# Kernel tuning notes

Hardware: AMD Instinct MI355X
Metric: run time of the kernel (lower is better)

Reference implementation:

```python
import jax, jax.numpy as jnp
import numpy as np

B, F, E, K, O = 4096, 64, 16, 8, 32
NFEAT, HID = 100000, 1024
EPS = 1e-5
N_ITER = 50  # entmax bisection iterations (entmax package default)


def entmax15(x):
    # alpha=1.5 entmax via bisection, faithful to EntmaxBisectFunction.forward
    d = x.shape[-1]
    xs = x * 0.5  # X * (alpha - 1)
    mx = jnp.max(xs, axis=-1, keepdims=True)
    tau_lo = mx - 1.0                      # gp(1, 1.5) = 1
    tau_hi = mx - (1.0 / d) ** 0.5         # gp(1/d, 1.5)
    f_lo = jnp.sum(jnp.square(jnp.maximum(xs - tau_lo, 0.0)), -1, keepdims=True) - 1.0
    dm = tau_hi - tau_lo

    def body(i, carry):
        tau_lo, dm, _ = carry
        dm = dm * 0.5
        tau_m = tau_lo + dm
        f_m = jnp.sum(jnp.square(jnp.maximum(xs - tau_m, 0.0)), -1, keepdims=True) - 1.0
        tau_lo = jnp.where(f_m * f_lo >= 0, tau_m, tau_lo)
        return (tau_lo, dm, tau_m)

    _, _, tau_m = jax.lax.fori_loop(0, N_ITER, body, (tau_lo, dm, tau_lo))
    p = jnp.square(jnp.maximum(xs - tau_m, 0.0))
    return p / jnp.sum(p, -1, keepdims=True)


def bn_channels(x, g, b):
    # BatchNorm1d on (B, C, L): normalize over batch and L per channel C (train mode)
    m = jnp.mean(x, (0, 2), keepdims=True)
    v = jnp.var(x, (0, 2), keepdims=True)
    return (x - m) / jnp.sqrt(v + EPS) * g[None, :, None] + b[None, :, None]


def bn_feat(x, g, b):
    # BatchNorm1d on (B, C) (train mode, biased variance)
    m = jnp.mean(x, 0)
    v = jnp.var(x, 0)
    return (x - m) / jnp.sqrt(v + EPS) * g + b


def setup_inputs() -> dict:
    key = jax.random.key(0)
    ks = jax.random.split(key, 12)
    gain = 1.414
    aQ = gain * np.sqrt(6.0 / (O + E))
    aB = gain * np.sqrt(6.0 / (E + E))
    aV = gain * np.sqrt(6.0 / (O + F))
    D0 = K * O * E
    return {
        'x_id': jax.random.randint(ks[0], (B, F), 0, NFEAT),
        'x_value': jax.random.uniform(ks[1], (B, F), dtype=jnp.float32),
        'emb': jax.random.normal(ks[2], (NFEAT, E), dtype=jnp.float32) * 0.1,
        'emb_g': jnp.ones((F,), jnp.float32), 'emb_b': jnp.zeros((F,), jnp.float32),
        'Q': jax.random.uniform(ks[3], (K, O, E), jnp.float32, -aQ, aQ),
        'bil': jax.random.uniform(ks[4], (K, E, E), jnp.float32, -aB, aB),
        'vals': jax.random.uniform(ks[5], (K, O, F), jnp.float32, -aV, aV),
        'arm_g': jnp.ones((K * O,), jnp.float32), 'arm_b': jnp.zeros((K * O,), jnp.float32),
        'w1': jax.random.normal(ks[6], (HID, D0), jnp.float32) / np.sqrt(D0),
        'b1': jnp.zeros((HID,), jnp.float32),
        'g1': jnp.ones((HID,), jnp.float32), 'bt1': jnp.zeros((HID,), jnp.float32),
        'w2': jax.random.normal(ks[7], (HID, HID), jnp.float32) / np.sqrt(HID),
        'b2': jnp.zeros((HID,), jnp.float32),
        'g2': jnp.ones((HID,), jnp.float32), 'bt2': jnp.zeros((HID,), jnp.float32),
        'wout': jax.random.normal(ks[8], (1, HID), jnp.float32) / np.sqrt(HID),
        'bout': jnp.zeros((1,), jnp.float32),
    }


def reference(x_id, x_value, emb, emb_g, emb_b, Q, bil, vals, arm_g, arm_b,
              w1, b1, g1, bt1, w2, b2, g2, bt2, wout, bout):
    v = jnp.clip(x_value, 0.001, 1.0)
    xe = emb[x_id] * v[..., None]                       # B,F,E
    x_exp = bn_channels(jnp.exp(xe), emb_g, emb_b)       # B,F,E
    # bilinear attention scores + global context bias
    kq = jnp.einsum('kxy,koy->kox', bil, Q)              # K,O,E (fuse param contraction)
    sc = jnp.einsum('bfx,kox->bkof', xe, kq)             # B,K,O,F
    gc = jnp.einsum('bx,kox->bko', xe.sum(1), kq)        # B,K,O
    sg = entmax15(sc + gc[..., None])                    # B,K,O,F sparse gates
    aw = sg * vals[None]                                 # B,K,O,F
    arm = jnp.einsum('bfe,bkof->bkoe', x_exp, aw)        # B,K,O,E
    arm = arm.reshape(arm.shape[0], K * O, E)
    arm = bn_channels(arm, arm_g, arm_b).reshape(arm.shape[0], -1)
    h = jax.nn.relu(bn_feat(arm @ w1.T + b1, g1, bt1))
    h = jax.nn.relu(bn_feat(h @ w2.T + b2, g2, bt2))
    y = h @ wout.T + bout
    return y[:, 0]
```

## Files before the change

### kernel.cpp

```cpp
#include <hip/hip_runtime.h>

#define EPS 1e-5f

typedef __bf16 bf16;
typedef bf16 bf16x8 __attribute__((ext_vector_type(8)));
typedef float f32x4 __attribute__((ext_vector_type(4)));
typedef float f32x2 __attribute__((ext_vector_type(2)));

__device__ __forceinline__ void lds_cp16(void* lds, const void* g) {
  __builtin_amdgcn_global_load_lds(
      (const __attribute__((address_space(1))) void*)g,
      (__attribute__((address_space(3))) void*)lds, 16, 0, 0);
}

__device__ __forceinline__ f32x4 mfma_bf16(bf16x8 a, bf16x8 b, f32x4 c) {
  return __builtin_amdgcn_mfma_f32_16x16x32_bf16(a, b, c, 0, 0, 0);
}

__global__ void k_zero(float* p) { p[blockIdx.x * 256 + threadIdx.x] = 0.0f; }

__global__ void k_embed(const int* __restrict__ x_id, const float* __restrict__ x_val,
                        const float* __restrict__ emb, float* __restrict__ xe) {
  int g = blockIdx.x * 256 + threadIdx.x;
  int id = x_id[g];
  float v = fminf(fmaxf(x_val[g], 0.001f), 1.0f);
  const float4* er = (const float4*)(emb + (size_t)id * 16);
  float4* xo = (float4*)(xe + (size_t)g * 16);
#pragma unroll
  for (int j = 0; j < 4; ++j) {
    float4 e = er[j];
    e.x *= v; e.y *= v; e.z *= v; e.w *= v;
    xo[j] = e;
  }
}

__global__ void k_expstats(const float* __restrict__ xe, float* __restrict__ es,
                           float* __restrict__ eq) {
  int t = threadIdx.x;
  int b0 = blockIdx.x * 16;
  float4 s4 = {0, 0, 0, 0}, q4 = {0, 0, 0, 0};
  for (int i = 0; i < 16; ++i) {
    float4 v = ((const float4*)(xe + (size_t)(b0 + i) * 1024))[t];
    float4 e;
    e.x = __expf(v.x); e.y = __expf(v.y); e.z = __expf(v.z); e.w = __expf(v.w);
    s4.x += e.x; s4.y += e.y; s4.z += e.z; s4.w += e.w;
    q4.x += e.x * e.x; q4.y += e.y * e.y; q4.z += e.z * e.z; q4.w += e.w * e.w;
  }
  float s = (s4.x + s4.y) + (s4.z + s4.w);
  float q = (q4.x + q4.y) + (q4.z + q4.w);
  s += __shfl_xor(s, 1, 64); s += __shfl_xor(s, 2, 64);
  q += __shfl_xor(q, 1, 64); q += __shfl_xor(q, 2, 64);
  if ((t & 3) == 0) {
    int f = t >> 2;
    atomicAdd(es + f, s);
    atomicAdd(eq + f, q);
  }
}

__global__ void k_expfin(const float* __restrict__ es, const float* __restrict__ eq,
                         const float* __restrict__ g_, const float* __restrict__ b_,
                         float* __restrict__ oa, float* __restrict__ ob) {
  int f = threadIdx.x;
  float mean = es[f] * (1.0f / 65536.0f);
  float var = eq[f] * (1.0f / 65536.0f) - mean * mean;
  float a = g_[f] * rsqrtf(var + EPS);
  oa[f] = a;
  ob[f] = b_[f] - mean * a;
}

__global__ void k_kq(const float* __restrict__ Qw, const float* __restrict__ bil,
                     float* __restrict__ kq) {
  int t = threadIdx.x;
  int k = t >> 5;
  float qv[16];
#pragma unroll
  for (int y = 0; y < 16; ++y) qv[y] = Qw[t * 16 + y];
  const float* bl = bil + k * 256;
#pragma unroll
  for (int x = 0; x < 16; ++x) {
    float s = 0.f;
#pragma unroll
    for (int y = 0; y < 16; ++y) s += bl[x * 16 + y] * qv[y];
    kq[t * 16 + x] = 0.5f * s;
  }
}

__global__ __launch_bounds__(256, 2) void k_attn(
    const float* __restrict__ xe_g, const float* __restrict__ kq_g,
    const float* __restrict__ eba, const float* __restrict__ ebb,
    const float* __restrict__ vals, bf16* __restrict__ arm) {
  __shared__ __align__(16) float s_xe[64 * 16];
  __shared__ float s_sum[16];
  __shared__ __align__(16) bf16 s_aw[256 * 72];
  __shared__ __align__(16) bf16 s_X[16 * 72];
  const int t = threadIdx.x;
  const int b = blockIdx.x;
  const f32x2 z2 = {0.f, 0.f};

  ((float4*)s_xe)[t] = ((const float4*)(xe_g + (size_t)b * 1024))[t];
  __syncthreads();

  if (t < 16) {
    float s = 0.f;
#pragma unroll
    for (int f = 0; f < 64; ++f) s += s_xe[f * 16 + t];
    s_sum[t] = s;
  }
  {
    int f = t >> 2, e0 = (t & 3) * 4;
    float a = eba[f], c = ebb[f];
#pragma unroll
    for (int j = 0; j < 4; ++j) {
      float v = __expf(s_xe[f * 16 + e0 + j]) * a + c;
      s_X[(e0 + j) * 72 + f] = (bf16)v;
    }
  }
  __syncthreads();

  f32x2 kq2[8];
  {
    const f32x4* g4 = (const f32x4*)(kq_g + t * 16);
#pragma unroll
    for (int j = 0; j < 4; ++j) {
      f32x4 v = g4[j];
      kq2[2 * j] = __builtin_shufflevector(v, v, 0, 1);
      kq2[2 * j + 1] = __builtin_shufflevector(v, v, 2, 3);
    }
  }
  float gc;
  {
    const f32x2* ss = (const f32x2*)s_sum;
    f32x2 g2 = z2;
#pragma unroll
    for (int i = 0; i < 8; ++i) g2 += ss[i] * kq2[i];
    gc = g2.x + g2.y;
  }

  f32x2 xs2[32];
#pragma unroll
  for (int f = 0; f < 64; ++f) {
    const f32x4* xr = (const f32x4*)(s_xe + f * 16);
    f32x4 A0 = xr[0], A1 = xr[1], A2 = xr[2], A3 = xr[3];
    f32x2 acc = z2;
    acc += __builtin_shufflevector(A0, A0, 0, 1) * kq2[0];
    acc += __builtin_shufflevector(A0, A0, 2, 3) * kq2[1];
    acc += __builtin_shufflevector(A1, A1, 0, 1) * kq2[2];
    acc += __builtin_shufflevector(A1, A1, 2, 3) * kq2[3];
    acc += __builtin_shufflevector(A2, A2, 0, 1) * kq2[4];
    acc += __builtin_shufflevector(A2, A2, 2, 3) * kq2[5];
    acc += __builtin_shufflevector(A3, A3, 0, 1) * kq2[6];
    acc += __builtin_shufflevector(A3, A3, 2, 3) * kq2[7];
    float v = (acc.x + acc.y) + gc;
    if (f & 1) xs2[f >> 1].y = v; else xs2[f >> 1].x = v;
  }

  f32x2 m2 = xs2[0];
#pragma unroll
  for (int i = 1; i < 32; ++i) m2 = __builtin_elementwise_max(m2, xs2[i]);
  float mx = fmaxf(m2.x, m2.y);

  float tau_lo = mx - 1.0f;
  float dm = 0.875f;
#pragma unroll
  for (int it = 0; it < 7; ++it) {
    dm *= 0.5f;
    float tm = tau_lo + dm;
    f32x2 t2 = {tm, tm};
    f32x2 c2 = z2;
#pragma unroll
    for (int i = 0; i < 32; ++i) {
      f32x2 d = xs2[i] - t2;
      d = __builtin_elementwise_max(d, z2);
      c2 += d * d;
    }
    tau_lo = ((c2.x + c2.y) - 1.0f >= 0.f) ? tm : tau_lo;
  }
  float tau = tau_lo + dm;
#pragma unroll
  for (int r = 0; r < 2; ++r) {
    f32x2 t2 = {tau, tau};
    f32x2 S2 = z2, Q2 = z2;
    float cnt = 0.f;
#pragma unroll
    for (int i = 0; i < 32; ++i) {
      f32x2 y = xs2[i] - t2;
      f32x2 m = __builtin_elementwise_max(y, z2);
      S2 += m; Q2 += m * m;
      cnt += (y.x > 0.f ? 1.f : 0.f) + (y.y > 0.f ? 1.f : 0.f);
    }
    float S1 = S2.x + S2.y, Q1 = Q2.x + Q2.y;
    float disc = fmaxf(S1 * S1 - cnt * (Q1 - 1.0f), 0.f);
    tau += (S1 - sqrtf(disc)) / cnt;
  }
  f32x2 Zv = z2;
  {
    f32x2 t2 = {tau, tau};
#pragma unroll
    for (int i = 0; i < 32; ++i) {
      f32x2 d = __builtin_elementwise_max(xs2[i] - t2, z2);
      f32x2 p = d * d;
      xs2[i] = p;
      Zv += p;
    }
  }
  float inv = 1.0f / (Zv.x + Zv.y);

  const float4* vg = (const float4*)(vals + t * 64);
#pragma unroll
  for (int f8 = 0; f8 < 64; f8 += 8) {
    float4 v0 = vg[f8 / 4], v1 = vg[f8 / 4 + 1];
    union { bf16 h[8]; uint4 u; } pk;
    pk.h[0] = (bf16)(xs2[f8 / 2].x * inv * v0.x);
    pk.h[1] = (bf16)(xs2[f8 / 2].y * inv * v0.y);
    pk.h[2] = (bf16)(xs2[f8 / 2 + 1].x * inv * v0.z);
    pk.h[3] = (bf16)(xs2[f8 / 2 + 1].y * inv * v0.w);
    pk.h[4] = (bf16)(xs2[f8 / 2 + 2].x * inv * v1.x);
    pk.h[5] = (bf16)(xs2[f8 / 2 + 2].y * inv * v1.y);
    pk.h[6] = (bf16)(xs2[f8 / 2 + 3].x * inv * v1.z);
    pk.h[7] = (bf16)(xs2[f8 / 2 + 3].y * inv * v1.w);
    *(uint4*)(s_aw + t * 72 + f8) = pk.u;
  }
  __syncthreads();

  const int w = t >> 6, lane = t & 63;
  f32x4 acc[4];
#pragma unroll
  for (int mt = 0; mt < 4; ++mt) acc[mt] = (f32x4){0.f, 0.f, 0.f, 0.f};
#pragma unroll
  for (int ks = 0; ks < 2; ++ks) {
    bf16x8 bfrag = *(const bf16x8*)(s_X + (lane & 15) * 72 + ks * 32 + (lane >> 4) * 8);
#pragma unroll
    for (int mt = 0; mt < 4; ++mt) {
      int row = (w * 4 + mt) * 16 + (lane & 15);
      bf16x8 afrag = *(const bf16x8*)(s_aw + row * 72 + ks * 32 + (lane >> 4) * 8);
      acc[mt] = mfma_bf16(afrag, bfrag, acc[mt]);
    }
  }
  bf16* armb = arm + (size_t)b * 4096;
#pragma unroll
  for (int mt = 0; mt < 4; ++mt) {
    int ko0 = (w * 4 + mt) * 16 + (lane >> 4) * 4;
#pragma unroll
    for (int r = 0; r < 4; ++r)
      armb[(ko0 + r) * 16 + (lane & 15)] = (bf16)acc[mt][r];
  }
}

__global__ void k_armstats(const bf16* __restrict__ arm, float* __restrict__ as_,
                           float* __restrict__ aq) {
  int t = threadIdx.x;
  int b0 = blockIdx.x * 16;
  float s = 0.f, q = 0.f;
  for (int i = 0; i < 16; ++i) {
    const bf16* p = arm + (size_t)(b0 + i) * 4096 + t * 16;
    bf16x8 v0 = *(const bf16x8*)p;
    bf16x8 v1 = *(const bf16x8*)(p + 8);
#pragma unroll
    for (int j = 0; j < 8; ++j) {
      float a = (float)v0[j], c = (float)v1[j];
      s += a + c; q += a * a + c * c;
    }
  }
  atomicAdd(as_ + t, s);
  atomicAdd(aq + t, q);
}

__global__ void k_armfin(const float* __restrict__ as_, const float* __restrict__ aq,
                         const float* __restrict__ g_, const float* __restrict__ b_,
                         float* __restrict__ oa, float* __restrict__ oc) {
  int ko = threadIdx.x;
  float mean = as_[ko] * (1.0f / 65536.0f);
  float var = aq[ko] * (1.0f / 65536.0f) - mean * mean;
  float a = g_[ko] * rsqrtf(var + EPS);
  oa[ko] = a;
  oc[ko] = b_[ko] - mean * a;
}

__global__ void k_cvtw1s(const float* __restrict__ s, const float* __restrict__ a,
                         bf16* __restrict__ d, int n4) {
  int stride = gridDim.x * 256;
  for (int i = blockIdx.x * 256 + threadIdx.x; i < n4; i += stride) {
    float4 v = ((const float4*)s)[i];
    float av = a[(i >> 2) & 255];
    union { bf16 h[4]; uint2 u; } p;
    p.h[0] = (bf16)(v.x * av); p.h[1] = (bf16)(v.y * av);
    p.h[2] = (bf16)(v.z * av); p.h[3] = (bf16)(v.w * av);
    *(uint2*)(d + (size_t)i * 4) = p.u;
  }
}

__global__ void k_bias1(const float* __restrict__ w1, const float* __restrict__ c,
                        const float* __restrict__ b1, float* __restrict__ bias1) {
  int t = threadIdx.x;
  int w = t >> 6, lane = t & 63;
  int h = blockIdx.x * 4 + w;
  const float4* row = (const float4*)(w1 + (size_t)h * 4096);
  float s = 0.f;
#pragma unroll
  for (int it = 0; it < 16; ++it) {
    int j4 = it * 64 + lane;
    float4 v = row[j4];
    float cj = c[j4 >> 2];
    s += cj * ((v.x + v.y) + (v.z + v.w));
  }
#pragma unroll
  for (int off = 32; off > 0; off >>= 1) s += __shfl_xor(s, off, 64);
  if (lane == 0) bias1[h] = b1[h] + s;
}

__global__ void k_cvt(const float* __restrict__ s, bf16* __restrict__ d, int n4) {
  int stride = gridDim.x * 256;
  for (int i = blockIdx.x * 256 + threadIdx.x; i < n4; i += stride) {
    float4 v = ((const float4*)s)[i];
    union { bf16 h[4]; uint2 u; } p;
    p.h[0] = (bf16)v.x; p.h[1] = (bf16)v.y; p.h[2] = (bf16)v.z; p.h[3] = (bf16)v.w;
    *(uint2*)(d + (size_t)i * 4) = p.u;
  }
}

__global__ __launch_bounds__(256, 2) void gemm_bt(
    const bf16* __restrict__ A, const bf16* __restrict__ Bw,
    const float* __restrict__ bias, float* __restrict__ C,
    float* __restrict__ csum, float* __restrict__ csq, int Kd) {
  __shared__ __align__(16) bf16 sA[128 * 32];
  __shared__ __align__(16) bf16 sB[64 * 32];
  const int t = threadIdx.x;
  const int w = t >> 6, lane = t & 63;
  const int m0 = blockIdx.x * 128, n0 = blockIdx.y * 64;

  f32x4 acc[2][4];
#pragma unroll
  for (int i = 0; i < 2; ++i)
#pragma unroll
    for (int j = 0; j < 4; ++j) acc[i][j] = (f32x4){0.f, 0.f, 0.f, 0.f};

  for (int kt = 0; kt < Kd; kt += 32) {
#pragma unroll
    for (int c = 0; c < 2; ++c) {
      int idx = c * 256 + t;
      int row = idx >> 2, ch = idx & 3;
      int sch = ch ^ ((row >> 1) & 3);
      lds_cp16(sA + idx * 8, A + (size_t)(m0 + row) * Kd + kt + sch * 8);
    }
    {
      int row = t >> 2, ch = t & 3;
      int sch = ch ^ ((row >> 1) & 3);
      lds_cp16(sB + t * 8, Bw + (size_t)(n0 + row) * Kd + kt + sch * 8);
    }
    __syncthreads();
    bf16x8 af[2], bfr[4];
#pragma unroll
    for (int mt = 0; mt < 2; ++mt) {
      int row = w * 32 + mt * 16 + (lane & 15);
      int ch = (lane >> 4) ^ ((row >> 1) & 3);
      af[mt] = *(const bf16x8*)(sA + row * 32 + ch * 8);
    }
#pragma unroll
    for (int nt = 0; nt < 4; ++nt) {
      int row = nt * 16 + (lane & 15);
      int ch = (lane >> 4) ^ ((row >> 1) & 3);
      bfr[nt] = *(const bf16x8*)(sB + row * 32 + ch * 8);
    }
#pragma unroll
    for (int mt = 0; mt < 2; ++mt)
#pragma unroll
      for (int nt = 0; nt < 4; ++nt)
        acc[mt][nt] = mfma_bf16(af[mt], bfr[nt], acc[mt][nt]);
    __syncthreads();
  }

#pragma unroll
  for (int nt = 0; nt < 4; ++nt) {
    int ncol = n0 + nt * 16 + (lane & 15);
    float bv = bias[ncol];
    float s = 0.f, q = 0.f;
#pragma unroll
    for (int mt = 0; mt < 2; ++mt) {
      int mr = m0 + w * 32 + mt * 16 + (lane >> 4) * 4;
#pragma unroll
      for (int r = 0; r < 4; ++r) {
        float v = acc[mt][nt][r] + bv;
        C[(size_t)(mr + r) * 1024 + ncol] = v;
        s += v; q += v * v;
      }
    }
    s += __shfl_xor(s, 16, 64); s += __shfl_xor(s, 32, 64);
    q += __shfl_xor(q, 16, 64); q += __shfl_xor(q, 32, 64);
    if ((lane >> 4) == 0) {
      atomicAdd(csum + ncol, s);
      atomicAdd(csq + ncol, q);
    }
  }
}

__global__ void k_colfin(const float* __restrict__ s, const float* __restrict__ q,
                         const float* __restrict__ g_, const float* __restrict__ bt,
                         float* __restrict__ a, float* __restrict__ c) {
  int h = blockIdx.x * 256 + threadIdx.x;
  float mean = s[h] * (1.0f / 4096.0f);
  float var = q[h] * (1.0f / 4096.0f) - mean * mean;
  float av = g_[h] * rsqrtf(var + EPS);
  a[h] = av;
  c[h] = bt[h] - mean * av;
}

__global__ void k_h1bf(const float* __restrict__ C1, const float* __restrict__ a,
                       const float* __restrict__ c, bf16* __restrict__ H1) {
  int i4 = blockIdx.x * 256 + threadIdx.x;
  int col0 = (i4 * 4) & 1023;
  float4 v = ((const float4*)C1)[i4];
  float4 av = *(const float4*)(a + col0);
  float4 cv = *(const float4*)(c + col0);
  union { bf16 h[4]; uint2 u; } pk;
  pk.h[0] = (bf16)fmaxf(v.x * av.x + cv.x, 0.f);
  pk.h[1] = (bf16)fmaxf(v.y * av.y + cv.y, 0.f);
  pk.h[2] = (bf16)fmaxf(v.z * av.z + cv.z, 0.f);
  pk.h[3] = (bf16)fmaxf(v.w * av.w + cv.w, 0.f);
  *(uint2*)(H1 + (size_t)i4 * 4) = pk.u;
}

__global__ __launch_bounds__(256) void k_out(const float* __restrict__ C2,
                                             const float* __restrict__ a,
                                             const float* __restrict__ c,
                                             const float* __restrict__ wout,
                                             const float* __restrict__ bout,
                                             float* __restrict__ y) {
  int t = threadIdx.x;
  int w = t >> 6, lane = t & 63;
  int row = blockIdx.x * 4 + w;
  const float* cr = C2 + (size_t)row * 1024;
  float s = 0.f;
#pragma unroll
  for (int j = 0; j < 16; ++j) {
    int col = j * 64 + lane;
    float v = fmaxf(cr[col] * a[col] + c[col], 0.f);
    s += v * wout[col];
  }
#pragma unroll
  for (int off = 32; off > 0; off >>= 1) s += __shfl_xor(s, off, 64);
  if (lane == 0) y[row] = s + bout[0];
}

extern "C" void kernel_launch(void* const* d_in, const int* in_sizes, int n_in,
                              void* d_out, int out_size, void* d_ws, size_t ws_size,
                              hipStream_t stream) {
  (void)in_sizes; (void)n_in; (void)out_size; (void)ws_size;
  const int* x_id = (const int*)d_in[0];
  const float* x_value = (const float*)d_in[1];
  const float* emb = (const float*)d_in[2];
  const float* emb_g = (const float*)d_in[3];
  const float* embb = (const float*)d_in[4];
  const float* Qw = (const float*)d_in[5];
  const float* bil = (const float*)d_in[6];
  const float* vals = (const float*)d_in[7];
  const float* arm_g = (const float*)d_in[8];
  const float* arm_b = (const float*)d_in[9];
  const float* w1 = (const float*)d_in[10];
  const float* b1 = (const float*)d_in[11];
  const float* g1 = (const float*)d_in[12];
  const float* bt1 = (const float*)d_in[13];
  const float* w2 = (const float*)d_in[14];
  const float* b2 = (const float*)d_in[15];
  const float* g2 = (const float*)d_in[16];
  const float* bt2 = (const float*)d_in[17];
  const float* wout = (const float*)d_in[18];
  const float* bout = (const float*)d_in[19];

  char* w = (char*)d_ws;
  float* ws_xe = (float*)w;
  float* ws_C = ws_xe;
  bf16* ws_arm = (bf16*)(w + 16777216);
  bf16* ws_H1 = (bf16*)(w + 50331648);
  bf16* ws_w1b = (bf16*)(w + 58720256);
  bf16* ws_w2b = (bf16*)(w + 67108864);
  float* ws_kq = (float*)(w + 69206016);
  float* st = (float*)(w + 69222400);
  float* es = st;
  float* eq = es + 64;
  float* as_ = eq + 64;
  float* aq = as_ + 256;
  float* s1 = aq + 256;
  float* q1 = s1 + 1024;
  float* s2 = q1 + 1024;
  float* q2 = s2 + 1024;
  float* eb_a = st + 5120;
  float* eb_b = eb_a + 64;
  float* arm_a = eb_b + 64;
  float* arm_c = arm_a + 256;
  float* a1c = arm_c + 256;
  float* c1c = a1c + 1024;
  float* a2c = c1c + 1024;
  float* c2c = a2c + 1024;
  float* bias1 = c2c + 1024;

  k_zero<<<20, 256, 0, stream>>>(st);
  k_embed<<<1024, 256, 0, stream>>>(x_id, x_value, emb, ws_xe);
  k_expstats<<<256, 256, 0, stream>>>(ws_xe, es, eq);
  k_expfin<<<1, 64, 0, stream>>>(es, eq, emb_g, embb, eb_a, eb_b);
  k_kq<<<1, 256, 0, stream>>>(Qw, bil, ws_kq);
  k_attn<<<4096, 256, 0, stream>>>(ws_xe, ws_kq, eb_a, eb_b, vals, ws_arm);
  k_armstats<<<256, 256, 0, stream>>>(ws_arm, as_, aq);
  k_armfin<<<1, 256, 0, stream>>>(as_, aq, arm_g, arm_b, arm_a, arm_c);
  k_cvtw1s<<<1024, 256, 0, stream>>>(w1, arm_a, ws_w1b, 1048576);
  k_bias1<<<256, 256, 0, stream>>>(w1, arm_c, b1, bias1);
  k_cvt<<<256, 256, 0, stream>>>(w2, ws_w2b, 262144);
  gemm_bt<<<dim3(32, 16), 256, 0, stream>>>(ws_arm, ws_w1b, bias1, ws_C, s1, q1, 4096);
  k_colfin<<<4, 256, 0, stream>>>(s1, q1, g1, bt1, a1c, c1c);
  k_h1bf<<<4096, 256, 0, stream>>>(ws_C, a1c, c1c, ws_H1);
  gemm_bt<<<dim3(32, 16), 256, 0, stream>>>(ws_H1, ws_w2b, b2, ws_C, s2, q2, 1024);
  k_colfin<<<4, 256, 0, stream>>>(s2, q2, g2, bt2, a2c, c2c);
  k_out<<<1024, 256, 0, stream>>>(ws_C, a2c, c2c, wout, bout, (float*)d_out);
}
```

Measured before the change: 358.1 us.

## Split-K GEMMs with 128x128 tiles, drop BN-cancelled biases, alias attn LDS

```diff
diff --git a/kernel.cpp b/kernel.cpp
--- a/kernel.cpp
+++ b/kernel.cpp
@@ -57,19 +57,11 @@
   }
 }
 
-__global__ void k_expfin(const float* __restrict__ es, const float* __restrict__ eq,
-                         const float* __restrict__ g_, const float* __restrict__ b_,
-                         float* __restrict__ oa, float* __restrict__ ob) {
-  int f = threadIdx.x;
-  float mean = es[f] * (1.0f / 65536.0f);
-  float var = eq[f] * (1.0f / 65536.0f) - mean * mean;
-  float a = g_[f] * rsqrtf(var + EPS);
-  oa[f] = a;
-  ob[f] = b_[f] - mean * a;
-}
-
-__global__ void k_kq(const float* __restrict__ Qw, const float* __restrict__ bil,
-                     float* __restrict__ kq) {
+__global__ void k_prep(const float* __restrict__ Qw, const float* __restrict__ bil,
+                       float* __restrict__ kq, const float* __restrict__ es,
+                       const float* __restrict__ eq, const float* __restrict__ g_,
+                       const float* __restrict__ b_, float* __restrict__ oa,
+                       float* __restrict__ ob) {
   int t = threadIdx.x;
   int k = t >> 5;
   float qv[16];
@@ -83,16 +75,24 @@
     for (int y = 0; y < 16; ++y) s += bl[x * 16 + y] * qv[y];
     kq[t * 16 + x] = 0.5f * s;
   }
-}
-
-__global__ __launch_bounds__(256, 2) void k_attn(
+  if (t < 64) {
+    float mean = es[t] * (1.0f / 65536.0f);
+    float var = eq[t] * (1.0f / 65536.0f) - mean * mean;
+    float a = g_[t] * rsqrtf(var + EPS);
+    oa[t] = a;
+    ob[t] = b_[t] - mean * a;
+  }
+}
+
+__global__ __launch_bounds__(256, 4) void k_attn(
     const float* __restrict__ xe_g, const float* __restrict__ kq_g,
     const float* __restrict__ eba, const float* __restrict__ ebb,
     const float* __restrict__ vals, bf16* __restrict__ arm) {
-  __shared__ __align__(16) float s_xe[64 * 16];
-  __shared__ float s_sum[16];
-  __shared__ __align__(16) bf16 s_aw[256 * 72];
-  __shared__ __align__(16) bf16 s_X[16 * 72];
+  __shared__ __align__(16) unsigned char smem[39168];
+  float* s_xe = (float*)smem;
+  float* s_sum = (float*)(smem + 4096);
+  bf16* s_aw = (bf16*)smem;
+  bf16* s_X = (bf16*)(smem + 36864);
   const int t = threadIdx.x;
   const int b = blockIdx.x;
   const f32x2 z2 = {0.f, 0.f};
@@ -153,6 +153,7 @@
     float v = (acc.x + acc.y) + gc;
     if (f & 1) xs2[f >> 1].y = v; else xs2[f >> 1].x = v;
   }
+  __syncthreads();
 
   f32x2 m2 = xs2[0];
 #pragma unroll
@@ -249,9 +250,9 @@
 __global__ void k_armstats(const bf16* __restrict__ arm, float* __restrict__ as_,
                            float* __restrict__ aq) {
   int t = threadIdx.x;
-  int b0 = blockIdx.x * 16;
+  int b0 = blockIdx.x * 8;
   float s = 0.f, q = 0.f;
-  for (int i = 0; i < 16; ++i) {
+  for (int i = 0; i < 8; ++i) {
     const bf16* p = arm + (size_t)(b0 + i) * 4096 + t * 16;
     bf16x8 v0 = *(const bf16x8*)p;
     bf16x8 v1 = *(const bf16x8*)(p + 8);
@@ -266,14 +267,11 @@
 }
 
 __global__ void k_armfin(const float* __restrict__ as_, const float* __restrict__ aq,
-                         const float* __restrict__ g_, const float* __restrict__ b_,
-                         float* __restrict__ oa, float* __restrict__ oc) {
+                         const float* __restrict__ g_, float* __restrict__ oa) {
   int ko = threadIdx.x;
   float mean = as_[ko] * (1.0f / 65536.0f);
   float var = aq[ko] * (1.0f / 65536.0f) - mean * mean;
-  float a = g_[ko] * rsqrtf(var + EPS);
-  oa[ko] = a;
-  oc[ko] = b_[ko] - mean * a;
+  oa[ko] = g_[ko] * rsqrtf(var + EPS);
 }
 
 __global__ void k_cvtw1s(const float* __restrict__ s, const float* __restrict__ a,
@@ -289,25 +287,6 @@
   }
 }
 
-__global__ void k_bias1(const float* __restrict__ w1, const float* __restrict__ c,
-                        const float* __restrict__ b1, float* __restrict__ bias1) {
-  int t = threadIdx.x;
-  int w = t >> 6, lane = t & 63;
-  int h = blockIdx.x * 4 + w;
-  const float4* row = (const float4*)(w1 + (size_t)h * 4096);
-  float s = 0.f;
-#pragma unroll
-  for (int it = 0; it < 16; ++it) {
-    int j4 = it * 64 + lane;
-    float4 v = row[j4];
-    float cj = c[j4 >> 2];
-    s += cj * ((v.x + v.y) + (v.z + v.w));
-  }
-#pragma unroll
-  for (int off = 32; off > 0; off >>= 1) s += __shfl_xor(s, off, 64);
-  if (lane == 0) bias1[h] = b1[h] + s;
-}
-
 __global__ void k_cvt(const float* __restrict__ s, bf16* __restrict__ d, int n4) {
   int stride = gridDim.x * 256;
   for (int i = blockIdx.x * 256 + threadIdx.x; i < n4; i += stride) {
@@ -318,19 +297,21 @@
   }
 }
 
-__global__ __launch_bounds__(256, 2) void gemm_bt(
+__global__ __launch_bounds__(256, 2) void gemm_sk(
     const bf16* __restrict__ A, const bf16* __restrict__ Bw,
-    const float* __restrict__ bias, float* __restrict__ C,
-    float* __restrict__ csum, float* __restrict__ csq, int Kd) {
+    float* __restrict__ P0, float* __restrict__ P1, int Ktot, int Kd) {
   __shared__ __align__(16) bf16 sA[128 * 32];
-  __shared__ __align__(16) bf16 sB[64 * 32];
+  __shared__ __align__(16) bf16 sB[128 * 32];
   const int t = threadIdx.x;
   const int w = t >> 6, lane = t & 63;
-  const int m0 = blockIdx.x * 128, n0 = blockIdx.y * 64;
-
-  f32x4 acc[2][4];
-#pragma unroll
-  for (int i = 0; i < 2; ++i)
+  const int m0 = blockIdx.x * 128, n0 = blockIdx.y * 128;
+  const int k0 = blockIdx.z * Kd;
+  float* P = blockIdx.z ? P1 : P0;
+  const int wr = (w >> 1) * 64, wc = (w & 1) * 64;
+
+  f32x4 acc[4][4];
+#pragma unroll
+  for (int i = 0; i < 4; ++i)
 #pragma unroll
     for (int j = 0; j < 4; ++j) acc[i][j] = (f32x4){0.f, 0.f, 0.f, 0.f};
 
@@ -340,29 +321,25 @@
       int idx = c * 256 + t;
       int row = idx >> 2, ch = idx & 3;
       int sch = ch ^ ((row >> 1) & 3);
-      lds_cp16(sA + idx * 8, A + (size_t)(m0 + row) * Kd + kt + sch * 8);
-    }
-    {
-      int row = t >> 2, ch = t & 3;
-      int sch = ch ^ ((row >> 1) & 3);
-      lds_cp16(sB + t * 8, Bw + (size_t)(n0 + row) * Kd + kt + sch * 8);
+      lds_cp16(sA + idx * 8, A + (size_t)(m0 + row) * Ktot + k0 + kt + sch * 8);
+      lds_cp16(sB + idx * 8, Bw + (size_t)(n0 + row) * Ktot + k0 + kt + sch * 8);
     }
     __syncthreads();
-    bf16x8 af[2], bfr[4];
-#pragma unroll
-    for (int mt = 0; mt < 2; ++mt) {
-      int row = w * 32 + mt * 16 + (lane & 15);
+    bf16x8 af[4], bfr[4];
+#pragma unroll
+    for (int mt = 0; mt < 4; ++mt) {
+      int row = wr + mt * 16 + (lane & 15);
       int ch = (lane >> 4) ^ ((row >> 1) & 3);
       af[mt] = *(const bf16x8*)(sA + row * 32 + ch * 8);
     }
 #pragma unroll
     for (int nt = 0; nt < 4; ++nt) {
-      int row = nt * 16 + (lane & 15);
+      int row = wc + nt * 16 + (lane & 15);
       int ch = (lane >> 4) ^ ((row >> 1) & 3);
       bfr[nt] = *(const bf16x8*)(sB + row * 32 + ch * 8);
     }
 #pragma unroll
-    for (int mt = 0; mt < 2; ++mt)
+    for (int mt = 0; mt < 4; ++mt)
 #pragma unroll
       for (int nt = 0; nt < 4; ++nt)
         acc[mt][nt] = mfma_bf16(af[mt], bfr[nt], acc[mt][nt]);
@@ -371,26 +348,35 @@
 
 #pragma unroll
   for (int nt = 0; nt < 4; ++nt) {
-    int ncol = n0 + nt * 16 + (lane & 15);
-    float bv = bias[ncol];
-    float s = 0.f, q = 0.f;
-#pragma unroll
-    for (int mt = 0; mt < 2; ++mt) {
-      int mr = m0 + w * 32 + mt * 16 + (lane >> 4) * 4;
-#pragma unroll
-      for (int r = 0; r < 4; ++r) {
-        float v = acc[mt][nt][r] + bv;
-        C[(size_t)(mr + r) * 1024 + ncol] = v;
-        s += v; q += v * v;
-      }
-    }
-    s += __shfl_xor(s, 16, 64); s += __shfl_xor(s, 32, 64);
-    q += __shfl_xor(q, 16, 64); q += __shfl_xor(q, 32, 64);
-    if ((lane >> 4) == 0) {
-      atomicAdd(csum + ncol, s);
-      atomicAdd(csq + ncol, q);
-    }
-  }
+    int ncol = n0 + wc + nt * 16 + (lane & 15);
+#pragma unroll
+    for (int mt = 0; mt < 4; ++mt) {
+      int mr = m0 + wr + mt * 16 + (lane >> 4) * 4;
+#pragma unroll
+      for (int r = 0; r < 4; ++r)
+        P[(size_t)(mr + r) * 1024 + ncol] = acc[mt][nt][r];
+    }
+  }
+}
+
+__global__ void k_colstats(const float* __restrict__ P0, const float* __restrict__ P1,
+                           float* __restrict__ cs, float* __restrict__ cq) {
+  int t = threadIdx.x;
+  int r0 = blockIdx.x * 16;
+  float4 s4 = {0, 0, 0, 0}, q4 = {0, 0, 0, 0};
+  for (int i = 0; i < 16; ++i) {
+    float4 a = ((const float4*)(P0 + (size_t)(r0 + i) * 1024))[t];
+    float4 b = ((const float4*)(P1 + (size_t)(r0 + i) * 1024))[t];
+    float4 v;
+    v.x = a.x + b.x; v.y = a.y + b.y; v.z = a.z + b.z; v.w = a.w + b.w;
+    s4.x += v.x; s4.y += v.y; s4.z += v.z; s4.w += v.w;
+    q4.x += v.x * v.x; q4.y += v.y * v.y; q4.z += v.z * v.z; q4.w += v.w * v.w;
+  }
+  int c0 = t * 4;
+  atomicAdd(cs + c0 + 0, s4.x); atomicAdd(cs + c0 + 1, s4.y);
+  atomicAdd(cs + c0 + 2, s4.z); atomicAdd(cs + c0 + 3, s4.w);
+  atomicAdd(cq + c0 + 0, q4.x); atomicAdd(cq + c0 + 1, q4.y);
+  atomicAdd(cq + c0 + 2, q4.z); atomicAdd(cq + c0 + 3, q4.w);
 }
 
 __global__ void k_colfin(const float* __restrict__ s, const float* __restrict__ q,
@@ -404,22 +390,25 @@
   c[h] = bt[h] - mean * av;
 }
 
-__global__ void k_h1bf(const float* __restrict__ C1, const float* __restrict__ a,
-                       const float* __restrict__ c, bf16* __restrict__ H1) {
+__global__ void k_h1bf(const float* __restrict__ P0, const float* __restrict__ P1,
+                       const float* __restrict__ a, const float* __restrict__ c,
+                       bf16* __restrict__ H1) {
   int i4 = blockIdx.x * 256 + threadIdx.x;
   int col0 = (i4 * 4) & 1023;
-  float4 v = ((const float4*)C1)[i4];
+  float4 u = ((const float4*)P0)[i4];
+  float4 v = ((const float4*)P1)[i4];
   float4 av = *(const float4*)(a + col0);
   float4 cv = *(const float4*)(c + col0);
   union { bf16 h[4]; uint2 u; } pk;
-  pk.h[0] = (bf16)fmaxf(v.x * av.x + cv.x, 0.f);
-  pk.h[1] = (bf16)fmaxf(v.y * av.y + cv.y, 0.f);
-  pk.h[2] = (bf16)fmaxf(v.z * av.z + cv.z, 0.f);
-  pk.h[3] = (bf16)fmaxf(v.w * av.w + cv.w, 0.f);
+  pk.h[0] = (bf16)fmaxf((u.x + v.x) * av.x + cv.x, 0.f);
+  pk.h[1] = (bf16)fmaxf((u.y + v.y) * av.y + cv.y, 0.f);
+  pk.h[2] = (bf16)fmaxf((u.z + v.z) * av.z + cv.z, 0.f);
+  pk.h[3] = (bf16)fmaxf((u.w + v.w) * av.w + cv.w, 0.f);
   *(uint2*)(H1 + (size_t)i4 * 4) = pk.u;
 }
 
-__global__ __launch_bounds__(256) void k_out(const float* __restrict__ C2,
+__global__ __launch_bounds__(256) void k_out(const float* __restrict__ P0,
+                                             const float* __restrict__ P1,
                                              const float* __restrict__ a,
                                              const float* __restrict__ c,
                                              const float* __restrict__ wout,
@@ -428,12 +417,13 @@
   int t = threadIdx.x;
   int w = t >> 6, lane = t & 63;
   int row = blockIdx.x * 4 + w;
-  const float* cr = C2 + (size_t)row * 1024;
+  const float* r0 = P0 + (size_t)row * 1024;
+  const float* r1 = P1 + (size_t)row * 1024;
   float s = 0.f;
 #pragma unroll
   for (int j = 0; j < 16; ++j) {
     int col = j * 64 + lane;
-    float v = fmaxf(cr[col] * a[col] + c[col], 0.f);
+    float v = fmaxf((r0[col] + r1[col]) * a[col] + c[col], 0.f);
     s += v * wout[col];
   }
 #pragma unroll
@@ -454,27 +444,24 @@
   const float* bil = (const float*)d_in[6];
   const float* vals = (const float*)d_in[7];
   const float* arm_g = (const float*)d_in[8];
-  const float* arm_b = (const float*)d_in[9];
   const float* w1 = (const float*)d_in[10];
-  const float* b1 = (const float*)d_in[11];
   const float* g1 = (const float*)d_in[12];
   const float* bt1 = (const float*)d_in[13];
   const float* w2 = (const float*)d_in[14];
-  const float* b2 = (const float*)d_in[15];
   const float* g2 = (const float*)d_in[16];
   const float* bt2 = (const float*)d_in[17];
   const float* wout = (const float*)d_in[18];
   const float* bout = (const float*)d_in[19];
 
   char* w = (char*)d_ws;
-  float* ws_xe = (float*)w;
-  float* ws_C = ws_xe;
+  float* ws_A = (float*)w;
   bf16* ws_arm = (bf16*)(w + 16777216);
-  bf16* ws_H1 = (bf16*)(w + 50331648);
-  bf16* ws_w1b = (bf16*)(w + 58720256);
-  bf16* ws_w2b = (bf16*)(w + 67108864);
-  float* ws_kq = (float*)(w + 69206016);
-  float* st = (float*)(w + 69222400);
+  float* ws_D = (float*)(w + 50331648);
+  bf16* ws_w1b = (bf16*)(w + 67108864);
+  bf16* ws_H1 = ws_w1b;
+  bf16* ws_w2b = (bf16*)(w + 75497472);
+  float* ws_kq = (float*)(w + 77594624);
+  float* st = (float*)(w + 77611008);
   float* es = st;
   float* eq = es + 64;
   float* as_ = eq + 64;
@@ -486,28 +473,26 @@
   float* eb_a = st + 5120;
   float* eb_b = eb_a + 64;
   float* arm_a = eb_b + 64;
-  float* arm_c = arm_a + 256;
-  float* a1c = arm_c + 256;
+  float* a1c = arm_a + 256;
   float* c1c = a1c + 1024;
   float* a2c = c1c + 1024;
   float* c2c = a2c + 1024;
-  float* bias1 = c2c + 1024;
 
   k_zero<<<20, 256, 0, stream>>>(st);
-  k_embed<<<1024, 256, 0, stream>>>(x_id, x_value, emb, ws_xe);
-  k_expstats<<<256, 256, 0, stream>>>(ws_xe, es, eq);
-  k_expfin<<<1, 64, 0, stream>>>(es, eq, emb_g, embb, eb_a, eb_b);
-  k_kq<<<1, 256, 0, stream>>>(Qw, bil, ws_kq);
-  k_attn<<<4096, 256, 0, stream>>>(ws_xe, ws_kq, eb_a, eb_b, vals, ws_arm);
-  k_armstats<<<256, 256, 0, stream>>>(ws_arm, as_, aq);
-  k_armfin<<<1, 256, 0, stream>>>(as_, aq, arm_g, arm_b, arm_a, arm_c);
+  k_embed<<<1024, 256, 0, stream>>>(x_id, x_value, emb, ws_A);
+  k_expstats<<<256, 256, 0, stream>>>(ws_A, es, eq);
+  k_prep<<<1, 256, 0, stream>>>(Qw, bil, ws_kq, es, eq, emb_g, embb, eb_a, eb_b);
+  k_attn<<<4096, 256, 0, stream>>>(ws_A, ws_kq, eb_a, eb_b, vals, ws_arm);
+  k_armstats<<<512, 256, 0, stream>>>(ws_arm, as_, aq);
+  k_armfin<<<1, 256, 0, stream>>>(as_, aq, arm_g, arm_a);
   k_cvtw1s<<<1024, 256, 0, stream>>>(w1, arm_a, ws_w1b, 1048576);
-  k_bias1<<<256, 256, 0, stream>>>(w1, arm_c, b1, bias1);
   k_cvt<<<256, 256, 0, stream>>>(w2, ws_w2b, 262144);
-  gemm_bt<<<dim3(32, 16), 256, 0, stream>>>(ws_arm, ws_w1b, bias1, ws_C, s1, q1, 4096);
+  gemm_sk<<<dim3(32, 8, 2), 256, 0, stream>>>(ws_arm, ws_w1b, ws_A, ws_D, 4096, 2048);
+  k_colstats<<<256, 256, 0, stream>>>(ws_A, ws_D, s1, q1);
   k_colfin<<<4, 256, 0, stream>>>(s1, q1, g1, bt1, a1c, c1c);
-  k_h1bf<<<4096, 256, 0, stream>>>(ws_C, a1c, c1c, ws_H1);
-  gemm_bt<<<dim3(32, 16), 256, 0, stream>>>(ws_H1, ws_w2b, b2, ws_C, s2, q2, 1024);
+  k_h1bf<<<4096, 256, 0, stream>>>(ws_A, ws_D, a1c, c1c, ws_H1);
+  gemm_sk<<<dim3(32, 8, 2), 256, 0, stream>>>(ws_H1, ws_w2b, ws_A, ws_D, 1024, 512);
+  k_colstats<<<256, 256, 0, stream>>>(ws_A, ws_D, s2, q2);
   k_colfin<<<4, 256, 0, stream>>>(s2, q2, g2, bt2, a2c, c2c);
-  k_out<<<1024, 256, 0, stream>>>(ws_C, a2c, c2c, wout, bout, (float*)d_out);
-}
+  k_out<<<1024, 256, 0, stream>>>(ws_A, ws_D, a2c, c2c, wout, bout, (float*)d_out);
+}
```

Measured after the change: 409.6 us. 1.14x slower.
